# Kernel tuning notes

Hardware: AMD Instinct MI355X
Metric: run time of the kernel (lower is better)

## Reference

```python
import jax, jax.numpy as jnp
import numpy as np

B, T_ENC, T_DEC = 64, 100, 50
L = 512      # lstm_size
E = 512      # input_encoding_size
H = 512      # att_hidden_size
R = 8        # num_review_steps
V_TOK = 30001  # token_cnt + 1 embedding rows
V_OUT = 30000  # word_cnt


def _lstm_maxout(s, c):
    # ARNet/neuraltalk2 LSTMCore: 5*L preactivations, maxout input transform
    i = jax.nn.sigmoid(s[:, :L])
    f = jax.nn.sigmoid(s[:, L:2 * L])
    o = jax.nn.sigmoid(s[:, 2 * L:3 * L])
    t = jnp.maximum(s[:, 3 * L:4 * L], s[:, 4 * L:])
    c2 = f * c + i * t
    return o * jnp.tanh(c2), c2


def _attend(feats, h, Wa2a, ba2a, Wh2a, bh2a, Watt, batt):
    # feats: [B, A, F], h: [B, L] -> context [B, F]
    p = jnp.tanh(feats @ Wa2a + ba2a + (h @ Wh2a + bh2a)[:, None, :])  # [B,A,H]
    e = jnp.squeeze(p @ Watt, -1) + batt                               # [B,A]
    a = jax.nn.softmax(e, axis=-1)
    return jnp.einsum('ba,baf->bf', a, feats)


def setup_inputs() -> dict:
    key = jax.random.key(0)
    ks = iter(jax.random.split(key, 48))
    g = lambda shape: jax.random.normal(next(ks), shape, jnp.float32) * 0.05
    z = lambda shape: jnp.zeros(shape, jnp.float32)
    return {
        'code_matrix': jax.random.randint(next(ks), (B, T_ENC), 0, V_TOK),
        'comment_matrix': jax.random.randint(next(ks), (B, T_DEC), 0, V_TOK),
        'current_comment_mask_cuda': jnp.ones((B, T_DEC), jnp.float32),
        'embed': jax.random.uniform(next(ks), (V_TOK, E), jnp.float32, -0.1, 0.1),
        'enc_Wi': g((E, 5 * L)), 'enc_bi': z((5 * L,)),
        'enc_Wh': g((L, 5 * L)), 'enc_bh': z((5 * L,)),
        'rev_Wh': g((R, L, 5 * L)), 'rev_bh': z((R, 5 * L)),
        'rev_Wa': g((R, L, 5 * L)), 'rev_ba': z((R, 5 * L)),
        'rev_Wa2a': g((R, L, H)), 'rev_ba2a': z((R, H)),
        'rev_Wh2a': g((R, L, H)), 'rev_bh2a': z((R, H)),
        'rev_Watt': g((R, H, 1)), 'rev_batt': z((R,)),
        'dec_Wi': g((E, 5 * L)), 'dec_bi': z((5 * L,)),
        'dec_Wh': g((L, 5 * L)), 'dec_bh': z((5 * L,)),
        'dec_Wa': g((L, 5 * L)), 'dec_ba': z((5 * L,)),
        'dec_Wa2a': g((L, H)), 'dec_ba2a': z((H,)),
        'dec_Wh2a': g((L, H)), 'dec_bh2a': z((H,)),
        'dec_Watt': g((H, 1)), 'dec_batt': z(()),
        'logit_W': jax.random.uniform(next(ks), (L, V_OUT), jnp.float32, -0.1, 0.1),
        'logit_b': z((V_OUT,)),
    }


def reference(code_matrix, comment_matrix, current_comment_mask_cuda, embed,
              enc_Wi, enc_bi, enc_Wh, enc_bh,
              rev_Wh, rev_bh, rev_Wa, rev_ba, rev_Wa2a, rev_ba2a,
              rev_Wh2a, rev_bh2a, rev_Watt, rev_batt,
              dec_Wi, dec_bi, dec_Wh, dec_bh, dec_Wa, dec_ba,
              dec_Wa2a, dec_ba2a, dec_Wh2a, dec_bh2a, dec_Watt, dec_batt,
              logit_W, logit_b):
    del current_comment_mask_cuda  # only used by scheduled sampling (ss_prob=0)
    Bsz = code_matrix.shape[0]
    h0 = jnp.zeros((Bsz, L), embed.dtype)
    c0 = jnp.zeros((Bsz, L), embed.dtype)

    # ---- encode ----
    enc_x = embed[code_matrix]  # [B, T_enc, E]

    def enc_step(carry, xt):
        h, c = carry
        s = xt @ enc_Wi + enc_bi + h @ enc_Wh + enc_bh
        h2, c2 = _lstm_maxout(s, c)
        return (h2, c2), h2

    (h_enc, c_enc), enc_hs = jax.lax.scan(enc_step, (h0, c0), jnp.swapaxes(enc_x, 0, 1))
    enc_hs = jnp.swapaxes(enc_hs, 0, 1)  # [B, T_enc, L]

    # ---- review (distinct params per step; scan over stacked params) ----
    def rev_step(carry, p):
        h, c = carry
        Wh, bh, Wa, ba, Wa2a, ba2a, Wh2a, bh2a, Watt, batt = p
        att_v = _attend(enc_hs, h, Wa2a, ba2a, Wh2a, bh2a, Watt, batt)
        s = h @ Wh + bh + att_v @ Wa + ba
        h2, c2 = _lstm_maxout(s, c)
        return (h2, c2), h2

    rev_params = (rev_Wh, rev_bh, rev_Wa, rev_ba, rev_Wa2a, rev_ba2a,
                  rev_Wh2a, rev_bh2a, rev_Watt, rev_batt)
    _, thought = jax.lax.scan(rev_step, (h_enc, c_enc), rev_params)
    thought = jnp.swapaxes(thought, 0, 1)  # [B, R, L]

    # ---- decode (teacher forcing; decode_state starts from encode_state) ----
    dec_x = embed[comment_matrix]  # [B, T_dec, E]

    def dec_step(carry, xt):
        h, c = carry
        att_v = _attend(thought, h, dec_Wa2a, dec_ba2a, dec_Wh2a, dec_bh2a, dec_Watt, dec_batt)
        s = xt @ dec_Wi + dec_bi + h @ dec_Wh + dec_bh + att_v @ dec_Wa + dec_ba
        h2, c2 = _lstm_maxout(s, c)
        logp = jax.nn.log_softmax(h2 @ logit_W + logit_b, axis=-1)
        return (h2, c2), logp

    _, logps = jax.lax.scan(dec_step, (h_enc, c_enc), jnp.swapaxes(dec_x, 0, 1))
    return jnp.swapaxes(logps, 0, 1)  # [B, T_dec, V_OUT]
```

## Files before the change

kernel.cpp:

```cpp
#include <hip/hip_runtime.h>
#include <math.h>
#include <stdint.h>

#define BB     64
#define TENC   100
#define TDEC   50
#define LDIM   512
#define EE     512
#define HDIM   512
#define FIVEL  2560
#define RSTEPS 8
#define VOUT   30000

typedef __attribute__((ext_vector_type(8))) short short8v;
typedef __attribute__((ext_vector_type(4))) float floatx4;

__device__ __forceinline__ float sigmoidf_(float x) { return 1.0f / (1.0f + __expf(-x)); }
__device__ __forceinline__ unsigned short f2bf(float x) {
    unsigned u = __float_as_uint(x);
    u += 0x7FFFu + ((u >> 16) & 1u);
    return (unsigned short)(u >> 16);
}
__device__ __forceinline__ float bf2f(unsigned short h) {
    return __uint_as_float(((unsigned)h) << 16);
}

__global__ __launch_bounds__(128)
void gather_embed(const float* __restrict__ embed, const int* __restrict__ tok,
                  int T, unsigned short* __restrict__ X)
{
    int m = blockIdx.x, t = m / BB, b = m % BB;
    const float* src = embed + (size_t)tok[b * T + t] * EE;
    float4 v = *(const float4*)(src + threadIdx.x * 4);
    ushort4 o = { f2bf(v.x), f2bf(v.y), f2bf(v.z), f2bf(v.w) };
    *(ushort4*)(X + (size_t)m * EE + threadIdx.x * 4) = o;
}

__global__ __launch_bounds__(256)
void conv_transpose(const float* __restrict__ W, unsigned short* __restrict__ WT,
                    int K, int N, int ldWT, int kofs)
{
    __shared__ float tile[32][33];
    int n0 = blockIdx.x * 32, k0 = blockIdx.y * 32;
    int tx = threadIdx.x & 31, ty = threadIdx.x >> 5;
    #pragma unroll
    for (int i = 0; i < 4; ++i) {
        int k = k0 + ty + i * 8, n = n0 + tx;
        tile[ty + i * 8][tx] = (n < N) ? W[(size_t)k * N + n] : 0.f;
    }
    __syncthreads();
    #pragma unroll
    for (int i = 0; i < 4; ++i) {
        int n = n0 + ty + i * 8, k = k0 + tx;
        if (n < N) WT[(size_t)n * ldWT + kofs + k] = f2bf(tile[tx][ty + i * 8]);
    }
}

__global__ __launch_bounds__(256)
void gemm_bf16(const unsigned short* __restrict__ A, const unsigned short* __restrict__ BT,
               const float* __restrict__ bias, float* __restrict__ C,
               unsigned short* __restrict__ Cb, int N, int K, long ldc, int remap)
{
    __shared__ unsigned short lds[2][128][32];
    const int tid  = threadIdx.x;
    const int wave = tid >> 6, lane = tid & 63;
    const int m0 = blockIdx.y * 128, n0 = blockIdx.x * 128;
    const int wr = wave >> 1, wc = wave & 1;

    floatx4 acc[4][4] = {};

    const int sr  = lane >> 2;
    const int scp = lane & 3;

    for (int k0 = 0; k0 < K; k0 += 32) {
        #pragma unroll
        for (int half = 0; half < 2; ++half) {
            int rbase = wave * 32 + half * 16;
            int r = rbase + sr;
            int c = scp ^ ((r >> 1) & 3);
            const unsigned short* ga = A + (size_t)(m0 + r) * K + k0 + c * 8;
            int nr = n0 + r; if (nr >= N) nr = 0;
            const unsigned short* gb = BT + (size_t)nr * K + k0 + c * 8;
            __builtin_amdgcn_global_load_lds(
                (const __attribute__((address_space(1))) void*)ga,
                (__attribute__((address_space(3))) void*)&lds[0][rbase][0], 16, 0, 0);
            __builtin_amdgcn_global_load_lds(
                (const __attribute__((address_space(1))) void*)gb,
                (__attribute__((address_space(3))) void*)&lds[1][rbase][0], 16, 0, 0);
        }
        __syncthreads();

        short8v af[4], bv[4];
        #pragma unroll
        for (int i = 0; i < 4; ++i) {
            int ra = wr * 64 + i * 16 + (lane & 15);
            int ca = (lane >> 4) ^ ((ra >> 1) & 3);
            af[i] = *(const short8v*)&lds[0][ra][ca * 8];
            int rb = wc * 64 + i * 16 + (lane & 15);
            int cb = (lane >> 4) ^ ((rb >> 1) & 3);
            bv[i] = *(const short8v*)&lds[1][rb][cb * 8];
        }
        #pragma unroll
        for (int i = 0; i < 4; ++i)
            #pragma unroll
            for (int j = 0; j < 4; ++j)
                acc[i][j] = __builtin_amdgcn_mfma_f32_16x16x32_bf16(af[i], bv[j], acc[i][j], 0, 0, 0);
        __syncthreads();
    }

    const int crow0 = m0 + wr * 64 + (lane >> 4) * 4;
    const int ccol0 = n0 + wc * 64 + (lane & 15);
    #pragma unroll
    for (int i = 0; i < 4; ++i) {
        #pragma unroll
        for (int j = 0; j < 4; ++j) {
            int col = ccol0 + j * 16;
            if (col < N) {
                float bval = bias ? bias[col] : 0.f;
                #pragma unroll
                for (int rr = 0; rr < 4; ++rr) {
                    int m = crow0 + i * 16 + rr;
                    long orow = m;
                    if (remap) { int t = m >> 6, b = m & 63; orow = (long)b * TDEC + t; }
                    float v = acc[i][j][rr] + bval;
                    if (Cb) Cb[orow * ldc + col] = f2bf(v);
                    else    C [orow * ldc + col] = v;
                }
            }
        }
    }
}

template<int NF, int MODE>
__global__ __launch_bounds__(256)
void smallgemm(const unsigned short* __restrict__ a0,
               const unsigned short* __restrict__ a1,
               const unsigned short* __restrict__ a2,
               const unsigned short* __restrict__ BT, int ldBT,
               const unsigned short* __restrict__ pre,
               const float* __restrict__ b0, const float* __restrict__ b1,
               const float* __restrict__ b2,
               const float* __restrict__ c_in, float* __restrict__ c_out,
               unsigned short* __restrict__ h_out, unsigned short* __restrict__ h_copy,
               float* __restrict__ f_out)
{
    __shared__ unsigned short Alds[64][128];
    __shared__ unsigned short Blds[NF * 16][128];
    const int tid = threadIdx.x;
    const int wave = tid >> 6, lane = tid & 63;
    const int c0 = blockIdx.x * 16;

    const unsigned short* segs[3] = {a0, a1, a2};
    const int nseg = a2 ? 3 : (a1 ? 2 : 1);
    const int NO = nseg * 4;

    floatx4 acc[NF];
    #pragma unroll
    for (int g = 0; g < NF; ++g) acc[g] = (floatx4){0.f, 0.f, 0.f, 0.f};

    short8v ra[4], rb[NF];

    #define LOAD_TILE(ot_) do {                                                \
        int seg_ = (ot_) >> 2, k0_ = ((ot_) & 3) * 128;                        \
        const unsigned short* A_ = segs[seg_];                                 \
        _Pragma("unroll")                                                      \
        for (int j = 0; j < 4; ++j) {                                          \
            int idx = tid + j * 256; int r = idx >> 4, ch = idx & 15;          \
            ra[j] = *(const short8v*)(A_ + (size_t)r * 512 + k0_ + ch * 8);    \
        }                                                                      \
        _Pragma("unroll")                                                      \
        for (int j = 0; j < NF; ++j) {                                         \
            int idx = tid + j * 256; int r = idx >> 4, ch = idx & 15;          \
            int grow = (r >> 4) * 512 + c0 + (r & 15);                         \
            rb[j] = *(const short8v*)(BT + (size_t)grow * ldBT + seg_ * 512 + k0_ + ch * 8); \
        }                                                                      \
    } while (0)

    LOAD_TILE(0);
    for (int ot = 0; ot < NO; ++ot) {
        __syncthreads();
        #pragma unroll
        for (int j = 0; j < 4; ++j) {
            int idx = tid + j * 256; int r = idx >> 4, ch = idx & 15;
            *(short8v*)&Alds[r][(ch ^ (r & 7)) * 8] = ra[j];
        }
        #pragma unroll
        for (int j = 0; j < NF; ++j) {
            int idx = tid + j * 256; int r = idx >> 4, ch = idx & 15;
            *(short8v*)&Blds[r][(ch ^ (r & 7)) * 8] = rb[j];
        }
        __syncthreads();
        if (ot + 1 < NO) LOAD_TILE(ot + 1);

        const int arow = wave * 16 + (lane & 15);
        const int q = lane >> 4;
        #pragma unroll
        for (int kk = 0; kk < 4; ++kk) {
            int ch = kk * 4 + q;
            short8v af = *(const short8v*)&Alds[arow][(ch ^ (arow & 7)) * 8];
            #pragma unroll
            for (int g = 0; g < NF; ++g) {
                int brow = g * 16 + (lane & 15);
                short8v bf = *(const short8v*)&Blds[brow][(ch ^ (brow & 7)) * 8];
                acc[g] = __builtin_amdgcn_mfma_f32_16x16x32_bf16(af, bf, acc[g], 0, 0, 0);
            }
        }
    }
    #undef LOAD_TILE

    const int m = wave * 16 + (lane >> 4) * 4;
    const int c = c0 + (lane & 15);
    if (MODE == 1) {
        float bv = b0 ? b0[c] : 0.f;
        #pragma unroll
        for (int rr = 0; rr < 4; ++rr)
            f_out[(size_t)(m + rr) * 512 + c] = acc[0][rr] + bv;
    } else {
        float bias[5];
        #pragma unroll
        for (int g = 0; g < 5; ++g) {
            float v = b0[g * 512 + c];
            if (b1) v += b1[g * 512 + c];
            if (b2) v += b2[g * 512 + c];
            bias[g] = v;
        }
        #pragma unroll
        for (int rr = 0; rr < 4; ++rr) {
            int row = m + rr;
            float s[5];
            #pragma unroll
            for (int g = 0; g < 5; ++g) {
                s[g] = acc[g][rr] + bias[g];
                if (pre) s[g] += bf2f(pre[(size_t)row * FIVEL + g * 512 + c]);
            }
            float ig = sigmoidf_(s[0]), fg = sigmoidf_(s[1]), og = sigmoidf_(s[2]);
            float tt = fmaxf(s[3], s[4]);
            float c2 = fg * c_in[(size_t)row * 512 + c] + ig * tt;
            float h2 = og * tanhf(c2);
            c_out[(size_t)row * 512 + c] = c2;
            unsigned short hb = f2bf(h2);
            h_out[(size_t)row * 512 + c] = hb;
            if (h_copy) h_copy[(size_t)row * 512 + c] = hb;
        }
    }
}

__global__ __launch_bounds__(256)
void attend(const unsigned short* __restrict__ proj, const float* __restrict__ hproj,
            const unsigned short* __restrict__ feats, const float* __restrict__ Watt,
            unsigned short* __restrict__ att_v, int A)
{
    __shared__ float hp[512];
    __shared__ float wa[512];
    __shared__ float ealpha[128];
    const int b = blockIdx.x;
    const int tid = threadIdx.x;
    for (int i = tid; i < 512; i += 256) { hp[i] = hproj[b * HDIM + i]; wa[i] = Watt[i]; }
    __syncthreads();
    const int wave = tid >> 6, lane = tid & 63;
    for (int a = wave; a < A; a += 4) {
        short8v pv = *(const short8v*)(proj + ((size_t)a * BB + b) * HDIM + lane * 8);
        float e = 0.f;
        #pragma unroll
        for (int j = 0; j < 8; ++j) {
            int hcol = lane * 8 + j;
            e += tanhf(bf2f((unsigned short)pv[j]) + hp[hcol]) * wa[hcol];
        }
        #pragma unroll
        for (int off = 32; off; off >>= 1) e += __shfl_xor(e, off);
        if (lane == 0) ealpha[a] = e;
    }
    __syncthreads();
    if (wave == 0) {
        float v1 = (lane < A) ? ealpha[lane] : -3.0e38f;
        float v2 = (lane + 64 < A) ? ealpha[lane + 64] : -3.0e38f;
        float m = fmaxf(v1, v2);
        #pragma unroll
        for (int off = 32; off; off >>= 1) m = fmaxf(m, __shfl_xor(m, off));
        float x1 = (lane < A) ? __expf(v1 - m) : 0.f;
        float x2 = (lane + 64 < A) ? __expf(v2 - m) : 0.f;
        float ssum = x1 + x2;
        #pragma unroll
        for (int off = 32; off; off >>= 1) ssum += __shfl_xor(ssum, off);
        float inv = 1.0f / ssum;
        if (lane < A) ealpha[lane] = x1 * inv;
        if (lane + 64 < A) ealpha[lane + 64] = x2 * inv;
    }
    __syncthreads();
    #pragma unroll
    for (int jj = 0; jj < 2; ++jj) {
        int l = tid + jj * 256;
        float acc = 0.f;
        for (int a = 0; a < A; ++a)
            acc += ealpha[a] * bf2f(feats[((size_t)a * BB + b) * LDIM + l]);
        att_v[(size_t)b * LDIM + l] = f2bf(acc);
    }
}

__global__ __launch_bounds__(256)
void log_softmax_(float* __restrict__ out)
{
    float* row = out + (size_t)blockIdx.x * VOUT;
    const int tid = threadIdx.x;
    float m = -3.0e38f, s = 0.f;
    for (int i = tid; i < VOUT / 4; i += 256) {
        float4 x = ((const float4*)row)[i];
        float xs[4] = {x.x, x.y, x.z, x.w};
        #pragma unroll
        for (int q = 0; q < 4; ++q) {
            float v = xs[q];
            if (v > m) { s = s * __expf(m - v) + 1.0f; m = v; }
            else       { s += __expf(v - m); }
        }
    }
    #pragma unroll
    for (int off = 32; off; off >>= 1) {
        float mo = __shfl_xor(m, off);
        float so = __shfl_xor(s, off);
        float mn = fmaxf(m, mo);
        s = s * __expf(m - mn) + so * __expf(mo - mn);
        m = mn;
    }
    __shared__ float ms[4], ss[4];
    const int wave = tid >> 6, lane = tid & 63;
    if (lane == 0) { ms[wave] = m; ss[wave] = s; }
    __syncthreads();
    float M2 = fmaxf(fmaxf(ms[0], ms[1]), fmaxf(ms[2], ms[3]));
    float S2 = ss[0] * __expf(ms[0] - M2) + ss[1] * __expf(ms[1] - M2) +
               ss[2] * __expf(ms[2] - M2) + ss[3] * __expf(ms[3] - M2);
    float lse = M2 + __logf(S2);
    for (int i = tid; i < VOUT / 4; i += 256) {
        float4 x = ((const float4*)row)[i];
        x.x -= lse; x.y -= lse; x.z -= lse; x.w -= lse;
        ((float4*)row)[i] = x;
    }
}

extern "C" void kernel_launch(void* const* d_in, const int* in_sizes, int n_in,
                              void* d_out_, int out_size, void* d_ws, size_t ws_size,
                              hipStream_t stream)
{
    const int*   code     = (const int*)  d_in[0];
    const int*   comment  = (const int*)  d_in[1];
    const float* embed    = (const float*)d_in[3];
    const float* enc_Wi   = (const float*)d_in[4];
    const float* enc_bi   = (const float*)d_in[5];
    const float* enc_Wh   = (const float*)d_in[6];
    const float* enc_bh   = (const float*)d_in[7];
    const float* rev_Wh   = (const float*)d_in[8];
    const float* rev_bh   = (const float*)d_in[9];
    const float* rev_Wa   = (const float*)d_in[10];
    const float* rev_ba   = (const float*)d_in[11];
    const float* rev_Wa2a = (const float*)d_in[12];
    const float* rev_ba2a = (const float*)d_in[13];
    const float* rev_Wh2a = (const float*)d_in[14];
    const float* rev_bh2a = (const float*)d_in[15];
    const float* rev_Watt = (const float*)d_in[16];
    const float* dec_Wi   = (const float*)d_in[18];
    const float* dec_bi   = (const float*)d_in[19];
    const float* dec_Wh   = (const float*)d_in[20];
    const float* dec_bh   = (const float*)d_in[21];
    const float* dec_Wa   = (const float*)d_in[22];
    const float* dec_ba   = (const float*)d_in[23];
    const float* dec_Wa2a = (const float*)d_in[24];
    const float* dec_ba2a = (const float*)d_in[25];
    const float* dec_Wh2a = (const float*)d_in[26];
    const float* dec_bh2a = (const float*)d_in[27];
    const float* dec_Watt = (const float*)d_in[28];
    const float* logit_W  = (const float*)d_in[30];
    const float* logit_b  = (const float*)d_in[31];
    float* out = (float*)d_out_;

    float* ws = (float*)d_ws;
    size_t off = 0;

    float* X = ws; off += 8192000;
    unsigned short* enc_pre_b = (unsigned short*)X;
    unsigned short* logit_WT  = (unsigned short*)X;

    float* U = ws + off; off += 2293760;
    unsigned short* WiT_enc    = (unsigned short*)U;
    unsigned short* enc_x_b    = (unsigned short*)(U + 655360);
    unsigned short* rev_proj_b = (unsigned short*)U;
    unsigned short* dec_h_b    = (unsigned short*)U;

    unsigned short* enc_hs_b = (unsigned short*)(ws + off); off += 1638400;
    unsigned short* encWhT   = (unsigned short*)(ws + off); off += 655360;
    unsigned short* revWcomb = (unsigned short*)(ws + off); off += 10485760;
    unsigned short* decWcomb = (unsigned short*)(ws + off); off += 1966080;
    unsigned short* revWT    = (unsigned short*)(ws + off); off += 1048576;
    unsigned short* decWT    = (unsigned short*)(ws + off); off += 131072;
    unsigned short* revWh2aT = (unsigned short*)(ws + off); off += 1048576;
    unsigned short* decWh2aT = (unsigned short*)(ws + off); off += 131072;
    unsigned short* dec_x_b  = (unsigned short*)(ws + off); off += 819200;
    unsigned short* thought_b= (unsigned short*)(ws + off); off += 131072;
    unsigned short* tproj_b  = (unsigned short*)(ws + off); off += 131072;
    unsigned short* h0_b     = (unsigned short*)(ws + off); off += 16384;
    unsigned short* hb0      = (unsigned short*)(ws + off); off += 16384;
    unsigned short* hb1      = (unsigned short*)(ws + off); off += 16384;
    unsigned short* attv_b   = (unsigned short*)(ws + off); off += 16384;
    float* cbuf[4];
    for (int i = 0; i < 4; ++i) { cbuf[i] = ws + off; off += 32768; }
    float* hproj = ws + off; off += 32768;
    if (ws_size < off * sizeof(float)) return;

    unsigned short* hb[2] = {hb0, hb1};
    const dim3 blk(256);

    hipMemsetAsync(cbuf[0], 0, (size_t)BB * LDIM * sizeof(float), stream);
    hipMemsetAsync(h0_b, 0, (size_t)BB * LDIM * sizeof(unsigned short), stream);

    gather_embed<<<TENC * BB, 128, 0, stream>>>(embed, code, TENC, enc_x_b);
    gather_embed<<<TDEC * BB, 128, 0, stream>>>(embed, comment, TDEC, dec_x_b);
    conv_transpose<<<dim3(80, 16), blk, 0, stream>>>(enc_Wi, WiT_enc, 512, FIVEL, 512, 0);
    conv_transpose<<<dim3(80, 16), blk, 0, stream>>>(enc_Wh, encWhT, 512, FIVEL, 512, 0);
    for (int r = 0; r < RSTEPS; ++r) {
        conv_transpose<<<dim3(80, 16), blk, 0, stream>>>(
            rev_Wh + (size_t)r * 1310720, revWcomb + (size_t)r * 2621440, 512, FIVEL, 1024, 0);
        conv_transpose<<<dim3(80, 16), blk, 0, stream>>>(
            rev_Wa + (size_t)r * 1310720, revWcomb + (size_t)r * 2621440, 512, FIVEL, 1024, 512);
        conv_transpose<<<dim3(16, 16), blk, 0, stream>>>(
            rev_Wa2a + (size_t)r * 262144, revWT + (size_t)r * 262144, 512, 512, 512, 0);
        conv_transpose<<<dim3(16, 16), blk, 0, stream>>>(
            rev_Wh2a + (size_t)r * 262144, revWh2aT + (size_t)r * 262144, 512, 512, 512, 0);
    }
    conv_transpose<<<dim3(80, 16), blk, 0, stream>>>(dec_Wi, decWcomb, 512, FIVEL, 1536, 0);
    conv_transpose<<<dim3(80, 16), blk, 0, stream>>>(dec_Wh, decWcomb, 512, FIVEL, 1536, 512);
    conv_transpose<<<dim3(80, 16), blk, 0, stream>>>(dec_Wa, decWcomb, 512, FIVEL, 1536, 1024);
    conv_transpose<<<dim3(16, 16), blk, 0, stream>>>(dec_Wa2a, decWT, 512, 512, 512, 0);
    conv_transpose<<<dim3(16, 16), blk, 0, stream>>>(dec_Wh2a, decWh2aT, 512, 512, 512, 0);

    gemm_bf16<<<dim3(FIVEL / 128, TENC * BB / 128), blk, 0, stream>>>(
        enc_x_b, WiT_enc, enc_bi, nullptr, enc_pre_b, FIVEL, EE, FIVEL, 0);

    for (int t = 0; t < TENC; ++t) {
        const unsigned short* hin = (t == 0) ? h0_b : enc_hs_b + (size_t)(t - 1) * 32768;
        smallgemm<5, 0><<<32, blk, 0, stream>>>(
            hin, nullptr, nullptr, encWhT, 512,
            enc_pre_b + (size_t)t * BB * FIVEL,
            enc_bh, nullptr, nullptr,
            cbuf[t & 1], cbuf[(t + 1) & 1],
            enc_hs_b + (size_t)t * 32768, nullptr, nullptr);
    }
    const unsigned short* h_enc = enc_hs_b + (size_t)(TENC - 1) * 32768;

    conv_transpose<<<dim3((VOUT + 31) / 32, 16), blk, 0, stream>>>(
        logit_W, logit_WT, 512, VOUT, 512, 0);

    const unsigned short* rh = h_enc;
    for (int r = 0; r < RSTEPS; ++r) {
        gemm_bf16<<<dim3(4, 50), blk, 0, stream>>>(
            enc_hs_b, revWT + (size_t)r * 262144, rev_ba2a + (size_t)r * HDIM,
            nullptr, rev_proj_b, HDIM, LDIM, HDIM, 0);
        smallgemm<1, 1><<<32, blk, 0, stream>>>(
            rh, nullptr, nullptr, revWh2aT + (size_t)r * 262144, 512,
            nullptr, rev_bh2a + (size_t)r * HDIM, nullptr, nullptr,
            nullptr, nullptr, nullptr, nullptr, hproj);
        attend<<<BB, blk, 0, stream>>>(rev_proj_b, hproj, enc_hs_b,
                                       rev_Watt + (size_t)r * HDIM, attv_b, TENC);
        const float* ci = (r == 0) ? cbuf[0] : cbuf[2 + ((r - 1) & 1)];
        smallgemm<5, 0><<<32, blk, 0, stream>>>(
            rh, attv_b, nullptr, revWcomb + (size_t)r * 2621440, 1024,
            nullptr, rev_bh + (size_t)r * FIVEL, rev_ba + (size_t)r * FIVEL, nullptr,
            ci, cbuf[2 + (r & 1)],
            hb[r & 1], thought_b + (size_t)r * 32768, nullptr);
        rh = hb[r & 1];
    }

    gemm_bf16<<<dim3(4, 4), blk, 0, stream>>>(
        thought_b, decWT, dec_ba2a, nullptr, tproj_b, HDIM, LDIM, HDIM, 0);

    const unsigned short* dh = h_enc;
    for (int t = 0; t < TDEC; ++t) {
        smallgemm<1, 1><<<32, blk, 0, stream>>>(
            dh, nullptr, nullptr, decWh2aT, 512,
            nullptr, dec_bh2a, nullptr, nullptr,
            nullptr, nullptr, nullptr, nullptr, hproj);
        attend<<<BB, blk, 0, stream>>>(tproj_b, hproj, thought_b, dec_Watt, attv_b, RSTEPS);
        const float* ci = (t == 0) ? cbuf[0] : cbuf[2 + ((t - 1) & 1)];
        smallgemm<5, 0><<<32, blk, 0, stream>>>(
            dec_x_b + (size_t)t * 32768, dh, attv_b, decWcomb, 1536,
            nullptr, dec_bi, dec_bh, dec_ba,
            ci, cbuf[2 + (t & 1)],
            hb[t & 1], dec_h_b + (size_t)t * 32768, nullptr);
        dh = hb[t & 1];
    }

    gemm_bf16<<<dim3((VOUT + 127) / 128, TDEC * BB / 128), blk, 0, stream>>>(
        dec_h_b, logit_WT, logit_b, out, nullptr, VOUT, LDIM, VOUT, 1);
    log_softmax_<<<TDEC * BB, blk, 0, stream>>>(out);
}
```

Measured before the change: 4.012 ms.

## Fuse attention projection into attend, batch review projections, precompute decoder inputs

The h-to-attention projection GEMM is merged into a new attfuse kernel that handles two batch rows per block, which removes one launch per recurrent step. All 8 review-step encoder projections are now computed in a single wide GEMM before the loop instead of one GEMM per step. The decoder input projection (x@Wi) moves out of the recurrence into one batched GEMM, so each per-step LSTM kernel now reads two 512-wide K segments instead of three. Weight transposes are batched through blockIdx.z, and tanhf is replaced with an exp-based fast approximation. The attfuse projection uses scalar FMAs over 32 blocks rather than MFMA, which could become the bottleneck for each step.

```diff
diff --git a/kernel.cpp b/kernel.cpp
--- a/kernel.cpp
+++ b/kernel.cpp
@@ -14,8 +14,35 @@
 
 typedef __attribute__((ext_vector_type(8))) short short8v;
 typedef __attribute__((ext_vector_type(4))) float floatx4;
+typedef unsigned short ushort_t;
+
+static const size_t OFF_A        = 0;
+static const size_t OFF_WIT_ENC  = 8192000;
+static const size_t OFF_ENCX     = 8847360;
+static const size_t OFF_LOGWT    = 0;
+static const size_t OFF_DECH     = 7680000;
+static const size_t OFF_DECPRE   = 8499200;
+static const size_t OFF_ENC_HS   = 13107200;
+static const size_t OFF_ENC_WHT  = 14745600;
+static const size_t OFF_REVWC    = 15400960;
+static const size_t OFF_DECWC    = 25886720;
+static const size_t OFF_WIT_DEC  = 27197440;
+static const size_t OFF_REVWT    = 27852800;
+static const size_t OFF_DECWT    = 28901376;
+static const size_t OFF_REVWH2AT = 29032448;
+static const size_t OFF_DECWH2AT = 30081024;
+static const size_t OFF_DECX     = 30212096;
+static const size_t OFF_THOUGHT  = 31031296;
+static const size_t OFF_TPROJ    = 31162368;
+static const size_t OFF_HB0      = 31293440;
+static const size_t OFF_HB1      = 31309824;
+static const size_t OFF_ATTV     = 31326208;
+static const size_t OFF_H0       = 31342592;
+static const size_t OFF_C0       = 31358976;
+static const size_t WS_TOTAL     = 31490048;
 
 __device__ __forceinline__ float sigmoidf_(float x) { return 1.0f / (1.0f + __expf(-x)); }
+__device__ __forceinline__ float tanh_fast(float x) { return 1.0f - 2.0f / (__expf(2.0f * x) + 1.0f); }
 __device__ __forceinline__ unsigned short f2bf(float x) {
     unsigned u = __float_as_uint(x);
     u += 0x7FFFu + ((u >> 16) & 1u);
@@ -27,7 +54,7 @@
 
 __global__ __launch_bounds__(128)
 void gather_embed(const float* __restrict__ embed, const int* __restrict__ tok,
-                  int T, unsigned short* __restrict__ X)
+                  int T, ushort_t* __restrict__ X)
 {
     int m = blockIdx.x, t = m / BB, b = m % BB;
     const float* src = embed + (size_t)tok[b * T + t] * EE;
@@ -37,9 +64,11 @@
 }
 
 __global__ __launch_bounds__(256)
-void conv_transpose(const float* __restrict__ W, unsigned short* __restrict__ WT,
-                    int K, int N, int ldWT, int kofs)
-{
+void conv_transpose(const float* __restrict__ W, ushort_t* __restrict__ WT,
+                    int N, int ldWT, int kofs, long Wz, long WTz)
+{
+    W  += (size_t)blockIdx.z * Wz;
+    WT += (size_t)blockIdx.z * WTz;
     __shared__ float tile[32][33];
     int n0 = blockIdx.x * 32, k0 = blockIdx.y * 32;
     int tx = threadIdx.x & 31, ty = threadIdx.x >> 5;
@@ -57,18 +86,17 @@
 }
 
 __global__ __launch_bounds__(256)
-void gemm_bf16(const unsigned short* __restrict__ A, const unsigned short* __restrict__ BT,
+void gemm_bf16(const ushort_t* __restrict__ A, const ushort_t* __restrict__ BT,
                const float* __restrict__ bias, float* __restrict__ C,
-               unsigned short* __restrict__ Cb, int N, int K, long ldc, int remap)
-{
-    __shared__ unsigned short lds[2][128][32];
+               ushort_t* __restrict__ Cb, int N, int K, long ldc, int remap)
+{
+    __shared__ ushort_t lds[2][128][32];
     const int tid  = threadIdx.x;
     const int wave = tid >> 6, lane = tid & 63;
     const int m0 = blockIdx.y * 128, n0 = blockIdx.x * 128;
     const int wr = wave >> 1, wc = wave & 1;
 
     floatx4 acc[4][4] = {};
-
     const int sr  = lane >> 2;
     const int scp = lane & 3;
 
@@ -78,9 +106,9 @@
             int rbase = wave * 32 + half * 16;
             int r = rbase + sr;
             int c = scp ^ ((r >> 1) & 3);
-            const unsigned short* ga = A + (size_t)(m0 + r) * K + k0 + c * 8;
+            const ushort_t* ga = A + (size_t)(m0 + r) * K + k0 + c * 8;
             int nr = n0 + r; if (nr >= N) nr = 0;
-            const unsigned short* gb = BT + (size_t)nr * K + k0 + c * 8;
+            const ushort_t* gb = BT + (size_t)nr * K + k0 + c * 8;
             __builtin_amdgcn_global_load_lds(
                 (const __attribute__((address_space(1))) void*)ga,
                 (__attribute__((address_space(3))) void*)&lds[0][rbase][0], 16, 0, 0);
@@ -131,45 +159,38 @@
     }
 }
 
-template<int NF, int MODE>
 __global__ __launch_bounds__(256)
-void smallgemm(const unsigned short* __restrict__ a0,
-               const unsigned short* __restrict__ a1,
-               const unsigned short* __restrict__ a2,
-               const unsigned short* __restrict__ BT, int ldBT,
-               const unsigned short* __restrict__ pre,
-               const float* __restrict__ b0, const float* __restrict__ b1,
-               const float* __restrict__ b2,
-               const float* __restrict__ c_in, float* __restrict__ c_out,
-               unsigned short* __restrict__ h_out, unsigned short* __restrict__ h_copy,
-               float* __restrict__ f_out)
-{
-    __shared__ unsigned short Alds[64][128];
-    __shared__ unsigned short Blds[NF * 16][128];
+void lstm_small(const ushort_t* __restrict__ a0,
+                const ushort_t* __restrict__ a1,
+                const ushort_t* __restrict__ BT, int ldBT,
+                const ushort_t* __restrict__ pre,
+                const float* __restrict__ b0, const float* __restrict__ b1,
+                const float* __restrict__ c_in, float* __restrict__ c_out,
+                ushort_t* __restrict__ h_out, ushort_t* __restrict__ h_copy)
+{
+    __shared__ ushort_t Alds[64][128];
+    __shared__ ushort_t Blds[80][128];
     const int tid = threadIdx.x;
     const int wave = tid >> 6, lane = tid & 63;
     const int c0 = blockIdx.x * 16;
 
-    const unsigned short* segs[3] = {a0, a1, a2};
-    const int nseg = a2 ? 3 : (a1 ? 2 : 1);
+    const ushort_t* segs[2] = {a0, a1};
+    const int nseg = a1 ? 2 : 1;
     const int NO = nseg * 4;
 
-    floatx4 acc[NF];
-    #pragma unroll
-    for (int g = 0; g < NF; ++g) acc[g] = (floatx4){0.f, 0.f, 0.f, 0.f};
-
-    short8v ra[4], rb[NF];
+    floatx4 acc[5] = {};
+    short8v ra[4], rb[5];
 
     #define LOAD_TILE(ot_) do {                                                \
         int seg_ = (ot_) >> 2, k0_ = ((ot_) & 3) * 128;                        \
-        const unsigned short* A_ = segs[seg_];                                 \
+        const ushort_t* A_ = segs[seg_];                                       \
         _Pragma("unroll")                                                      \
         for (int j = 0; j < 4; ++j) {                                          \
             int idx = tid + j * 256; int r = idx >> 4, ch = idx & 15;          \
             ra[j] = *(const short8v*)(A_ + (size_t)r * 512 + k0_ + ch * 8);    \
         }                                                                      \
         _Pragma("unroll")                                                      \
-        for (int j = 0; j < NF; ++j) {                                         \
+        for (int j = 0; j < 5; ++j) {                                          \
             int idx = tid + j * 256; int r = idx >> 4, ch = idx & 15;          \
             int grow = (r >> 4) * 512 + c0 + (r & 15);                         \
             rb[j] = *(const short8v*)(BT + (size_t)grow * ldBT + seg_ * 512 + k0_ + ch * 8); \
@@ -185,7 +206,7 @@
             *(short8v*)&Alds[r][(ch ^ (r & 7)) * 8] = ra[j];
         }
         #pragma unroll
-        for (int j = 0; j < NF; ++j) {
+        for (int j = 0; j < 5; ++j) {
             int idx = tid + j * 256; int r = idx >> 4, ch = idx & 15;
             *(short8v*)&Blds[r][(ch ^ (r & 7)) * 8] = rb[j];
         }
@@ -199,7 +220,7 @@
             int ch = kk * 4 + q;
             short8v af = *(const short8v*)&Alds[arow][(ch ^ (arow & 7)) * 8];
             #pragma unroll
-            for (int g = 0; g < NF; ++g) {
+            for (int g = 0; g < 5; ++g) {
                 int brow = g * 16 + (lane & 15);
                 short8v bf = *(const short8v*)&Blds[brow][(ch ^ (brow & 7)) * 8];
                 acc[g] = __builtin_amdgcn_mfma_f32_16x16x32_bf16(af, bf, acc[g], 0, 0, 0);
@@ -210,90 +231,120 @@
 
     const int m = wave * 16 + (lane >> 4) * 4;
     const int c = c0 + (lane & 15);
-    if (MODE == 1) {
-        float bv = b0 ? b0[c] : 0.f;
-        #pragma unroll
-        for (int rr = 0; rr < 4; ++rr)
-            f_out[(size_t)(m + rr) * 512 + c] = acc[0][rr] + bv;
-    } else {
-        float bias[5];
+    float bias[5];
+    #pragma unroll
+    for (int g = 0; g < 5; ++g) {
+        float v = b0[g * 512 + c];
+        if (b1) v += b1[g * 512 + c];
+        bias[g] = v;
+    }
+    #pragma unroll
+    for (int rr = 0; rr < 4; ++rr) {
+        int row = m + rr;
+        float s[5];
         #pragma unroll
         for (int g = 0; g < 5; ++g) {
-            float v = b0[g * 512 + c];
-            if (b1) v += b1[g * 512 + c];
-            if (b2) v += b2[g * 512 + c];
-            bias[g] = v;
-        }
-        #pragma unroll
-        for (int rr = 0; rr < 4; ++rr) {
-            int row = m + rr;
-            float s[5];
+            s[g] = acc[g][rr] + bias[g];
+            if (pre) s[g] += bf2f(pre[(size_t)row * FIVEL + g * 512 + c]);
+        }
+        float ig = sigmoidf_(s[0]), fg = sigmoidf_(s[1]), og = sigmoidf_(s[2]);
+        float tt = fmaxf(s[3], s[4]);
+        float c2 = fg * c_in[(size_t)row * 512 + c] + ig * tt;
+        float h2 = og * tanh_fast(c2);
+        c_out[(size_t)row * 512 + c] = c2;
+        ushort_t hb_ = f2bf(h2);
+        h_out[(size_t)row * 512 + c] = hb_;
+        if (h_copy) h_copy[(size_t)row * 512 + c] = hb_;
+    }
+}
+
+__global__ __launch_bounds__(256)
+void attfuse(const ushort_t* __restrict__ hprev,
+             const ushort_t* __restrict__ projBase, long projLd,
+             const ushort_t* __restrict__ feats,
+             const ushort_t* __restrict__ W2aT, const float* __restrict__ b2a,
+             const float* __restrict__ Watt, ushort_t* __restrict__ attv,
+             int A)
+{
+    __shared__ ushort_t hl[2][512];
+    __shared__ float hp[2][512];
+    __shared__ float wa[512];
+    __shared__ float ealpha[2][128];
+    const int b0 = blockIdx.x * 2;
+    const int tid = threadIdx.x;
+    {
+        int i4 = tid * 4;
+        int bi = i4 >> 9, k = i4 & 511;
+        *(ushort4*)&hl[bi][k] = *(const ushort4*)(hprev + (size_t)(b0 + bi) * 512 + k);
+        wa[tid] = Watt[tid];
+        wa[tid + 256] = Watt[tid + 256];
+    }
+    __syncthreads();
+    #pragma unroll
+    for (int half = 0; half < 2; ++half) {
+        int n = tid + half * 256;
+        float a0 = b2a[n], a1 = a0;
+        const ushort_t* wrow = W2aT + (size_t)n * 512;
+        #pragma unroll 4
+        for (int k8 = 0; k8 < 64; ++k8) {
+            short8v w  = *(const short8v*)(wrow + k8 * 8);
+            short8v h0 = *(const short8v*)&hl[0][k8 * 8];
+            short8v h1 = *(const short8v*)&hl[1][k8 * 8];
             #pragma unroll
-            for (int g = 0; g < 5; ++g) {
-                s[g] = acc[g][rr] + bias[g];
-                if (pre) s[g] += bf2f(pre[(size_t)row * FIVEL + g * 512 + c]);
+            for (int e = 0; e < 8; ++e) {
+                float wf = bf2f((ushort_t)w[e]);
+                a0 += wf * bf2f((ushort_t)h0[e]);
+                a1 += wf * bf2f((ushort_t)h1[e]);
             }
-            float ig = sigmoidf_(s[0]), fg = sigmoidf_(s[1]), og = sigmoidf_(s[2]);
-            float tt = fmaxf(s[3], s[4]);
-            float c2 = fg * c_in[(size_t)row * 512 + c] + ig * tt;
-            float h2 = og * tanhf(c2);
-            c_out[(size_t)row * 512 + c] = c2;
-            unsigned short hb = f2bf(h2);
-            h_out[(size_t)row * 512 + c] = hb;
-            if (h_copy) h_copy[(size_t)row * 512 + c] = hb;
-        }
-    }
-}
-
-__global__ __launch_bounds__(256)
-void attend(const unsigned short* __restrict__ proj, const float* __restrict__ hproj,
-            const unsigned short* __restrict__ feats, const float* __restrict__ Watt,
-            unsigned short* __restrict__ att_v, int A)
-{
-    __shared__ float hp[512];
-    __shared__ float wa[512];
-    __shared__ float ealpha[128];
-    const int b = blockIdx.x;
-    const int tid = threadIdx.x;
-    for (int i = tid; i < 512; i += 256) { hp[i] = hproj[b * HDIM + i]; wa[i] = Watt[i]; }
+        }
+        hp[0][n] = a0;
+        hp[1][n] = a1;
+    }
     __syncthreads();
     const int wave = tid >> 6, lane = tid & 63;
-    for (int a = wave; a < A; a += 4) {
-        short8v pv = *(const short8v*)(proj + ((size_t)a * BB + b) * HDIM + lane * 8);
+    for (int idx = wave; idx < 2 * A; idx += 4) {
+        int a = idx >> 1, bi = idx & 1;
+        short8v pv = *(const short8v*)(projBase + ((size_t)a * 64 + b0 + bi) * projLd + lane * 8);
         float e = 0.f;
         #pragma unroll
         for (int j = 0; j < 8; ++j) {
-            int hcol = lane * 8 + j;
-            e += tanhf(bf2f((unsigned short)pv[j]) + hp[hcol]) * wa[hcol];
+            int h = lane * 8 + j;
+            e += tanh_fast(bf2f((ushort_t)pv[j]) + hp[bi][h]) * wa[h];
         }
         #pragma unroll
         for (int off = 32; off; off >>= 1) e += __shfl_xor(e, off);
-        if (lane == 0) ealpha[a] = e;
+        if (lane == 0) ealpha[bi][a] = e;
     }
     __syncthreads();
-    if (wave == 0) {
-        float v1 = (lane < A) ? ealpha[lane] : -3.0e38f;
-        float v2 = (lane + 64 < A) ? ealpha[lane + 64] : -3.0e38f;
-        float m = fmaxf(v1, v2);
-        #pragma unroll
-        for (int off = 32; off; off >>= 1) m = fmaxf(m, __shfl_xor(m, off));
-        float x1 = (lane < A) ? __expf(v1 - m) : 0.f;
-        float x2 = (lane + 64 < A) ? __expf(v2 - m) : 0.f;
-        float ssum = x1 + x2;
-        #pragma unroll
-        for (int off = 32; off; off >>= 1) ssum += __shfl_xor(ssum, off);
-        float inv = 1.0f / ssum;
-        if (lane < A) ealpha[lane] = x1 * inv;
-        if (lane + 64 < A) ealpha[lane + 64] = x2 * inv;
+    if (wave < 2) {
+        int bi = wave;
+        float v1 = (lane < A) ? ealpha[bi][lane] : -3.0e38f;
+        float v2 = (lane + 64 < A) ? ealpha[bi][lane + 64] : -3.0e38f;
+        float mm = fmaxf(v1, v2);
+        #pragma unroll
+        for (int off = 32; off; off >>= 1) mm = fmaxf(mm, __shfl_xor(mm, off));
+        float x1 = (lane < A) ? __expf(v1 - mm) : 0.f;
+        float x2 = (lane + 64 < A) ? __expf(v2 - mm) : 0.f;
+        float ss = x1 + x2;
+        #pragma unroll
+        for (int off = 32; off; off >>= 1) ss += __shfl_xor(ss, off);
+        float inv = 1.f / ss;
+        if (lane < A) ealpha[bi][lane] = x1 * inv;
+        if (lane + 64 < A) ealpha[bi][lane + 64] = x2 * inv;
     }
     __syncthreads();
     #pragma unroll
-    for (int jj = 0; jj < 2; ++jj) {
-        int l = tid + jj * 256;
-        float acc = 0.f;
-        for (int a = 0; a < A; ++a)
-            acc += ealpha[a] * bf2f(feats[((size_t)a * BB + b) * LDIM + l]);
-        att_v[(size_t)b * LDIM + l] = f2bf(acc);
+    for (int bi = 0; bi < 2; ++bi) {
+        int b = b0 + bi;
+        float s0 = 0.f, s1 = 0.f;
+        for (int a = 0; a < A; ++a) {
+            float al = ealpha[bi][a];
+            unsigned int u = *(const unsigned int*)(feats + ((size_t)a * 64 + b) * 512 + tid * 2);
+            s0 += al * bf2f((ushort_t)(u & 0xffffu));
+            s1 += al * bf2f((ushort_t)(u >> 16));
+        }
+        ushort2 o = { f2bf(s0), f2bf(s1) };
+        *(ushort2*)(attv + (size_t)b * 512 + tid * 2) = o;
     }
 }
 
@@ -372,117 +423,103 @@
     float* out = (float*)d_out_;
 
     float* ws = (float*)d_ws;
-    size_t off = 0;
-
-    float* X = ws; off += 8192000;
-    unsigned short* enc_pre_b = (unsigned short*)X;
-    unsigned short* logit_WT  = (unsigned short*)X;
-
-    float* U = ws + off; off += 2293760;
-    unsigned short* WiT_enc    = (unsigned short*)U;
-    unsigned short* enc_x_b    = (unsigned short*)(U + 655360);
-    unsigned short* rev_proj_b = (unsigned short*)U;
-    unsigned short* dec_h_b    = (unsigned short*)U;
-
-    unsigned short* enc_hs_b = (unsigned short*)(ws + off); off += 1638400;
-    unsigned short* encWhT   = (unsigned short*)(ws + off); off += 655360;
-    unsigned short* revWcomb = (unsigned short*)(ws + off); off += 10485760;
-    unsigned short* decWcomb = (unsigned short*)(ws + off); off += 1966080;
-    unsigned short* revWT    = (unsigned short*)(ws + off); off += 1048576;
-    unsigned short* decWT    = (unsigned short*)(ws + off); off += 131072;
-    unsigned short* revWh2aT = (unsigned short*)(ws + off); off += 1048576;
-    unsigned short* decWh2aT = (unsigned short*)(ws + off); off += 131072;
-    unsigned short* dec_x_b  = (unsigned short*)(ws + off); off += 819200;
-    unsigned short* thought_b= (unsigned short*)(ws + off); off += 131072;
-    unsigned short* tproj_b  = (unsigned short*)(ws + off); off += 131072;
-    unsigned short* h0_b     = (unsigned short*)(ws + off); off += 16384;
-    unsigned short* hb0      = (unsigned short*)(ws + off); off += 16384;
-    unsigned short* hb1      = (unsigned short*)(ws + off); off += 16384;
-    unsigned short* attv_b   = (unsigned short*)(ws + off); off += 16384;
+    if (ws_size < WS_TOTAL * sizeof(float)) return;
+
+    ushort_t* enc_pre_b = (ushort_t*)(ws + OFF_A);
+    ushort_t* rev_projA = (ushort_t*)(ws + OFF_A);
+    ushort_t* logit_WT  = (ushort_t*)(ws + OFF_LOGWT);
+    ushort_t* dec_h_b   = (ushort_t*)(ws + OFF_DECH);
+    ushort_t* dec_pre_b = (ushort_t*)(ws + OFF_DECPRE);
+    ushort_t* WiT_enc   = (ushort_t*)(ws + OFF_WIT_ENC);
+    ushort_t* enc_x_b   = (ushort_t*)(ws + OFF_ENCX);
+    ushort_t* enc_hs_b  = (ushort_t*)(ws + OFF_ENC_HS);
+    ushort_t* encWhT    = (ushort_t*)(ws + OFF_ENC_WHT);
+    ushort_t* revWcomb  = (ushort_t*)(ws + OFF_REVWC);
+    ushort_t* decWcomb  = (ushort_t*)(ws + OFF_DECWC);
+    ushort_t* WiT_dec   = (ushort_t*)(ws + OFF_WIT_DEC);
+    ushort_t* revWT     = (ushort_t*)(ws + OFF_REVWT);
+    ushort_t* decWT     = (ushort_t*)(ws + OFF_DECWT);
+    ushort_t* revWh2aT  = (ushort_t*)(ws + OFF_REVWH2AT);
+    ushort_t* decWh2aT  = (ushort_t*)(ws + OFF_DECWH2AT);
+    ushort_t* dec_x_b   = (ushort_t*)(ws + OFF_DECX);
+    ushort_t* thought_b = (ushort_t*)(ws + OFF_THOUGHT);
+    ushort_t* tproj_b   = (ushort_t*)(ws + OFF_TPROJ);
+    ushort_t* hb[2] = { (ushort_t*)(ws + OFF_HB0), (ushort_t*)(ws + OFF_HB1) };
+    ushort_t* attv_b    = (ushort_t*)(ws + OFF_ATTV);
+    ushort_t* h0_b      = (ushort_t*)(ws + OFF_H0);
     float* cbuf[4];
-    for (int i = 0; i < 4; ++i) { cbuf[i] = ws + off; off += 32768; }
-    float* hproj = ws + off; off += 32768;
-    if (ws_size < off * sizeof(float)) return;
-
-    unsigned short* hb[2] = {hb0, hb1};
+    for (int i = 0; i < 4; ++i) cbuf[i] = ws + OFF_C0 + (size_t)i * 32768;
+
     const dim3 blk(256);
 
     hipMemsetAsync(cbuf[0], 0, (size_t)BB * LDIM * sizeof(float), stream);
-    hipMemsetAsync(h0_b, 0, (size_t)BB * LDIM * sizeof(unsigned short), stream);
+    hipMemsetAsync(h0_b, 0, (size_t)BB * LDIM * sizeof(ushort_t), stream);
 
     gather_embed<<<TENC * BB, 128, 0, stream>>>(embed, code, TENC, enc_x_b);
     gather_embed<<<TDEC * BB, 128, 0, stream>>>(embed, comment, TDEC, dec_x_b);
-    conv_transpose<<<dim3(80, 16), blk, 0, stream>>>(enc_Wi, WiT_enc, 512, FIVEL, 512, 0);
-    conv_transpose<<<dim3(80, 16), blk, 0, stream>>>(enc_Wh, encWhT, 512, FIVEL, 512, 0);
-    for (int r = 0; r < RSTEPS; ++r) {
-        conv_transpose<<<dim3(80, 16), blk, 0, stream>>>(
-            rev_Wh + (size_t)r * 1310720, revWcomb + (size_t)r * 2621440, 512, FIVEL, 1024, 0);
-        conv_transpose<<<dim3(80, 16), blk, 0, stream>>>(
-            rev_Wa + (size_t)r * 1310720, revWcomb + (size_t)r * 2621440, 512, FIVEL, 1024, 512);
-        conv_transpose<<<dim3(16, 16), blk, 0, stream>>>(
-            rev_Wa2a + (size_t)r * 262144, revWT + (size_t)r * 262144, 512, 512, 512, 0);
-        conv_transpose<<<dim3(16, 16), blk, 0, stream>>>(
-            rev_Wh2a + (size_t)r * 262144, revWh2aT + (size_t)r * 262144, 512, 512, 512, 0);
-    }
-    conv_transpose<<<dim3(80, 16), blk, 0, stream>>>(dec_Wi, decWcomb, 512, FIVEL, 1536, 0);
-    conv_transpose<<<dim3(80, 16), blk, 0, stream>>>(dec_Wh, decWcomb, 512, FIVEL, 1536, 512);
-    conv_transpose<<<dim3(80, 16), blk, 0, stream>>>(dec_Wa, decWcomb, 512, FIVEL, 1536, 1024);
-    conv_transpose<<<dim3(16, 16), blk, 0, stream>>>(dec_Wa2a, decWT, 512, 512, 512, 0);
-    conv_transpose<<<dim3(16, 16), blk, 0, stream>>>(dec_Wh2a, decWh2aT, 512, 512, 512, 0);
+    conv_transpose<<<dim3(80, 16, 1), blk, 0, stream>>>(enc_Wi, WiT_enc, FIVEL, 512, 0, 0, 0);
+    conv_transpose<<<dim3(80, 16, 1), blk, 0, stream>>>(enc_Wh, encWhT, FIVEL, 512, 0, 0, 0);
+    conv_transpose<<<dim3(80, 16, 8), blk, 0, stream>>>(rev_Wh, revWcomb, FIVEL, 1024, 0,   1310720, 2621440);
+    conv_transpose<<<dim3(80, 16, 8), blk, 0, stream>>>(rev_Wa, revWcomb, FIVEL, 1024, 512, 1310720, 2621440);
+    conv_transpose<<<dim3(16, 16, 8), blk, 0, stream>>>(rev_Wa2a, revWT, 512, 512, 0,       262144, 262144);
+    conv_transpose<<<dim3(16, 16, 8), blk, 0, stream>>>(rev_Wh2a, revWh2aT, 512, 512, 0,    262144, 262144);
+    conv_transpose<<<dim3(80, 16, 1), blk, 0, stream>>>(dec_Wi, WiT_dec, FIVEL, 512, 0, 0, 0);
+    conv_transpose<<<dim3(80, 16, 1), blk, 0, stream>>>(dec_Wh, decWcomb, FIVEL, 1024, 0, 0, 0);
+    conv_transpose<<<dim3(80, 16, 1), blk, 0, stream>>>(dec_Wa, decWcomb, FIVEL, 1024, 512, 0, 0);
+    conv_transpose<<<dim3(16, 16, 1), blk, 0, stream>>>(dec_Wa2a, decWT, 512, 512, 0, 0, 0);
+    conv_transpose<<<dim3(16, 16, 1), blk, 0, stream>>>(dec_Wh2a, decWh2aT, 512, 512, 0, 0, 0);
 
     gemm_bf16<<<dim3(FIVEL / 128, TENC * BB / 128), blk, 0, stream>>>(
         enc_x_b, WiT_enc, enc_bi, nullptr, enc_pre_b, FIVEL, EE, FIVEL, 0);
 
     for (int t = 0; t < TENC; ++t) {
-        const unsigned short* hin = (t == 0) ? h0_b : enc_hs_b + (size_t)(t - 1) * 32768;
-        smallgemm<5, 0><<<32, blk, 0, stream>>>(
-            hin, nullptr, nullptr, encWhT, 512,
-            enc_pre_b + (size_t)t * BB * FIVEL,
-            enc_bh, nullptr, nullptr,
+        const ushort_t* hin = (t == 0) ? h0_b : enc_hs_b + (size_t)(t - 1) * 32768;
+        lstm_small<<<32, blk, 0, stream>>>(
+            hin, nullptr, encWhT, 512,
+            enc_pre_b + (size_t)t * 163840,
+            enc_bh, nullptr,
             cbuf[t & 1], cbuf[(t + 1) & 1],
-            enc_hs_b + (size_t)t * 32768, nullptr, nullptr);
-    }
-    const unsigned short* h_enc = enc_hs_b + (size_t)(TENC - 1) * 32768;
-
-    conv_transpose<<<dim3((VOUT + 31) / 32, 16), blk, 0, stream>>>(
-        logit_W, logit_WT, 512, VOUT, 512, 0);
-
-    const unsigned short* rh = h_enc;
+            enc_hs_b + (size_t)t * 32768, nullptr);
+    }
+    const ushort_t* h_enc = enc_hs_b + (size_t)(TENC - 1) * 32768;
+
+    gemm_bf16<<<dim3(32, 50), blk, 0, stream>>>(
+        enc_hs_b, revWT, rev_ba2a, nullptr, rev_projA, 4096, LDIM, 4096, 0);
+
+    const ushort_t* rh = h_enc;
     for (int r = 0; r < RSTEPS; ++r) {
-        gemm_bf16<<<dim3(4, 50), blk, 0, stream>>>(
-            enc_hs_b, revWT + (size_t)r * 262144, rev_ba2a + (size_t)r * HDIM,
-            nullptr, rev_proj_b, HDIM, LDIM, HDIM, 0);
-        smallgemm<1, 1><<<32, blk, 0, stream>>>(
-            rh, nullptr, nullptr, revWh2aT + (size_t)r * 262144, 512,
-            nullptr, rev_bh2a + (size_t)r * HDIM, nullptr, nullptr,
-            nullptr, nullptr, nullptr, nullptr, hproj);
-        attend<<<BB, blk, 0, stream>>>(rev_proj_b, hproj, enc_hs_b,
-                                       rev_Watt + (size_t)r * HDIM, attv_b, TENC);
+        attfuse<<<32, blk, 0, stream>>>(
+            rh, rev_projA + (size_t)r * 512, 4096, enc_hs_b,
+            revWh2aT + (size_t)r * 262144, rev_bh2a + (size_t)r * 512,
+            rev_Watt + (size_t)r * 512, attv_b, TENC);
         const float* ci = (r == 0) ? cbuf[0] : cbuf[2 + ((r - 1) & 1)];
-        smallgemm<5, 0><<<32, blk, 0, stream>>>(
-            rh, attv_b, nullptr, revWcomb + (size_t)r * 2621440, 1024,
-            nullptr, rev_bh + (size_t)r * FIVEL, rev_ba + (size_t)r * FIVEL, nullptr,
+        lstm_small<<<32, blk, 0, stream>>>(
+            rh, attv_b, revWcomb + (size_t)r * 2621440, 1024,
+            nullptr, rev_bh + (size_t)r * FIVEL, rev_ba + (size_t)r * FIVEL,
             ci, cbuf[2 + (r & 1)],
-            hb[r & 1], thought_b + (size_t)r * 32768, nullptr);
+            hb[r & 1], thought_b + (size_t)r * 32768);
         rh = hb[r & 1];
     }
 
     gemm_bf16<<<dim3(4, 4), blk, 0, stream>>>(
         thought_b, decWT, dec_ba2a, nullptr, tproj_b, HDIM, LDIM, HDIM, 0);
-
-    const unsigned short* dh = h_enc;
+    conv_transpose<<<dim3((VOUT + 31) / 32, 16, 1), blk, 0, stream>>>(
+        logit_W, logit_WT, VOUT, 512, 0, 0, 0);
+    gemm_bf16<<<dim3(FIVEL / 128, TDEC * BB / 128), blk, 0, stream>>>(
+        dec_x_b, WiT_dec, dec_bi, nullptr, dec_pre_b, FIVEL, EE, FIVEL, 0);
+
+    const ushort_t* dh = h_enc;
     for (int t = 0; t < TDEC; ++t) {
-        smallgemm<1, 1><<<32, blk, 0, stream>>>(
-            dh, nullptr, nullptr, decWh2aT, 512,
-            nullptr, dec_bh2a, nullptr, nullptr,
-            nullptr, nullptr, nullptr, nullptr, hproj);
-        attend<<<BB, blk, 0, stream>>>(tproj_b, hproj, thought_b, dec_Watt, attv_b, RSTEPS);
+        attfuse<<<32, blk, 0, stream>>>(
+            dh, tproj_b, 512, thought_b,
+            decWh2aT, dec_bh2a, dec_Watt, attv_b, RSTEPS);
         const float* ci = (t == 0) ? cbuf[0] : cbuf[2 + ((t - 1) & 1)];
-        smallgemm<5, 0><<<32, blk, 0, stream>>>(
-            dec_x_b + (size_t)t * 32768, dh, attv_b, decWcomb, 1536,
-            nullptr, dec_bi, dec_bh, dec_ba,
+        lstm_small<<<32, blk, 0, stream>>>(
+            dh, attv_b, decWcomb, 1024,
+            dec_pre_b + (size_t)t * 163840,
+            dec_bh, dec_ba,
             ci, cbuf[2 + (t & 1)],
-            hb[t & 1], dec_h_b + (size_t)t * 32768, nullptr);
+            hb[t & 1], dec_h_b + (size_t)t * 32768);
         dh = hb[t & 1];
     }
 
```

Result: slower. 4.592 ms (+14.5%).
